# Kernel optimization log

Measured on AMD Instinct MI355X. Metric: run time of the kernel, lower is better.

Reference implementation:

```python
import jax, jax.numpy as jnp
import numpy as np

B, L, E, D, H, N_ENT = 64, 50, 50, 100, 100, 200000


def setup_inputs() -> dict:
    key = jax.random.key(0)
    ks = jax.random.split(key, 12)
    neighbor_ids = jax.random.randint(ks[0], (B, L, E), 0, N_ENT)
    # 0/1 adjacency; mimic GraphConstructer: symmetric with self-loops
    adj = jax.random.randint(ks[1], (B, L, E, E), 0, 2).astype(jnp.int32)
    adj = jnp.maximum(adj, adj.transpose(0, 1, 3, 2))
    adj = jnp.maximum(adj, jnp.eye(E, dtype=jnp.int32))
    s = 0.1  # ~ 1/sqrt(D) init scale
    emb = jax.random.normal(ks[2], (N_ENT, D), jnp.float32) * s
    Wq = jax.random.normal(ks[3], (D, H), jnp.float32) * s
    bq = jax.random.normal(ks[4], (H,), jnp.float32) * s
    Wk = jax.random.normal(ks[5], (D, H), jnp.float32) * s
    bk = jax.random.normal(ks[6], (H,), jnp.float32) * s
    Wv = jax.random.normal(ks[7], (D, H), jnp.float32) * s
    bv = jax.random.normal(ks[8], (H,), jnp.float32) * s
    Ws = jax.random.normal(ks[9], (D, H), jnp.float32) * s
    bs = jax.random.normal(ks[10], (H,), jnp.float32) * s
    return {"neighbor_ids": neighbor_ids, "adj": adj, "emb": emb,
            "Wq": Wq, "bq": bq, "Wk": Wk, "bk": bk,
            "Wv": Wv, "bv": bv, "Ws": Ws, "bs": bs}


def reference(neighbor_ids, adj, emb, Wq, bq, Wk, bk, Wv, bv, Ws, bs):
    b, l, e = neighbor_ids.shape
    d = emb.shape[1]
    h = Wq.shape[1]
    # embedding gather: [B,L,E,D] -> [G,E,D], G = B*L graphs
    x = emb[neighbor_ids].reshape(b * l, e, d)
    a = adj.reshape(b * l, e, e)
    # TransformerConv (heads=1): q,k,v linear with bias
    q = x @ Wq + bq
    k = x @ Wk + bk
    v = x @ Wv + bv
    scores = jnp.einsum('gid,gjd->gij', q, k) / jnp.sqrt(jnp.asarray(h, x.dtype))
    # edge (j -> i) exists when adj[j, i] != 0; target i attends over sources j
    mask = a.transpose(0, 2, 1) != 0  # mask[g, i, j]
    neg = jnp.finfo(scores.dtype).min
    attn = jax.nn.softmax(jnp.where(mask, scores, neg), axis=-1)
    # nodes with no incoming edge aggregate to zero (PyG softmax/scatter semantics)
    attn = jnp.where(mask.any(-1, keepdims=True), attn, jnp.zeros((), attn.dtype))
    agg = jnp.einsum('gij,gjd->gid', attn, v)
    out = agg + x @ Ws + bs  # root/skip connection with bias
    # take center node (index 0) of each ego-graph -> [B, L, H]
    return out.reshape(b, l, e, h)[:, :, 0, :]
```

## Files before the change

### kernel.cpp

```cpp
#include <hip/hip_runtime.h>
#include <math.h>

#define E_N 50
#define D_N 100
#define H_N 100
#define XSTR 51
#define NTHR 256
#define GATHER_IT ((E_N * (D_N / 4) + NTHR - 1) / NTHR)

__device__ __forceinline__ float bf2f(unsigned int s16) {
    return __uint_as_float(s16 << 16);
}

__device__ __forceinline__ unsigned short f2bf(float f) {
    unsigned int u = __float_as_uint(f);
    unsigned int r = (u + 0x7FFFu + ((u >> 16) & 1u)) >> 16;
    return (unsigned short)r;
}

template <bool F32>
__device__ __forceinline__ float ldx(const void* p, int i) {
    if (F32) return reinterpret_cast<const float*>(p)[i];
    return bf2f(reinterpret_cast<const unsigned short*>(p)[i]);
}

template <bool F32>
__device__ __forceinline__ float4 ld4(const void* p, long long i4) {
    if (F32) return reinterpret_cast<const float4*>(p)[i4];
    uint2 v = reinterpret_cast<const uint2*>(p)[i4];
    float4 f;
    f.x = bf2f(v.x & 0xFFFFu);
    f.y = bf2f(v.x >> 16);
    f.z = bf2f(v.y & 0xFFFFu);
    f.w = bf2f(v.y >> 16);
    return f;
}

template <bool F32>
__device__ __forceinline__ void graph_core(
    int g, int tid, int mk, const int* idr,
    const void* __restrict__ emb,
    const void* __restrict__ Wq, const void* __restrict__ bq,
    const void* __restrict__ Wk, const void* __restrict__ Wv,
    const void* __restrict__ bv, const void* __restrict__ Ws,
    const void* __restrict__ bs, void* __restrict__ out,
    float* xs, float* q0s, float* us, float* attns, float* ys, float* den_s)
{
    #pragma unroll
    for (int r = 0; r < GATHER_IT; ++r) {
        int i = tid + NTHR * r;
        if (i < E_N * (D_N / 4)) {
            int j  = i / 25;
            int d4 = i - j * 25;
            float4 v = ld4<F32>(emb, (long long)idr[r] * (D_N / 4) + d4);
            int d0 = d4 * 4;
            xs[(d0 + 0) * XSTR + j] = v.x;
            xs[(d0 + 1) * XSTR + j] = v.y;
            xs[(d0 + 2) * XSTR + j] = v.z;
            xs[(d0 + 3) * XSTR + j] = v.w;
        }
    }
    __syncthreads();

    if (tid < H_N) {
        float acc = ldx<F32>(bq, tid);
        #pragma unroll 10
        for (int d = 0; d < D_N; ++d)
            acc = fmaf(xs[d * XSTR], ldx<F32>(Wq, d * H_N + tid), acc);
        q0s[tid] = acc;
    }
    __syncthreads();

    if (tid < D_N) {
        float a0 = 0.f, a1 = 0.f, a2 = 0.f, a3 = 0.f;
        const float4* q4 = reinterpret_cast<const float4*>(q0s);
        #pragma unroll 5
        for (int h4 = 0; h4 < H_N / 4; ++h4) {
            float4 w = ld4<F32>(Wk, (long long)tid * (H_N / 4) + h4);
            float4 q = q4[h4];
            a0 = fmaf(w.x, q.x, a0);
            a1 = fmaf(w.y, q.y, a1);
            a2 = fmaf(w.z, q.z, a2);
            a3 = fmaf(w.w, q.w, a3);
        }
        us[tid] = (a0 + a1) + (a2 + a3);
    }
    __syncthreads();

    if (tid < 64) {
        float s = 0.f;
        if (tid < E_N) {
            #pragma unroll 10
            for (int d = 0; d < D_N; ++d)
                s = fmaf(us[d], xs[d * XSTR + tid], s);
            s *= 0.1f;
        }
        bool live = (tid < E_N) && (mk != 0);
        float m = live ? s : -3.0e38f;
        #pragma unroll
        for (int off = 32; off; off >>= 1)
            m = fmaxf(m, __shfl_xor(m, off));
        float e = live ? __expf(s - m) : 0.f;
        float den = e;
        #pragma unroll
        for (int off = 32; off; off >>= 1)
            den += __shfl_xor(den, off);
        float inv = den > 0.f ? 1.0f / den : 0.f;
        if (tid < E_N) attns[tid] = e * inv;
        if (tid == 0)  *den_s = den;
    }
    __syncthreads();

    if (tid < D_N) {
        float acc = 0.f;
        #pragma unroll 10
        for (int j = 0; j < E_N; ++j)
            acc = fmaf(attns[j], xs[tid * XSTR + j], acc);
        ys[tid] = acc;
    }
    __syncthreads();

    if (tid < H_N) {
        float sflag = *den_s > 0.f ? 1.f : 0.f;
        float acc = ldx<F32>(bs, tid) + ldx<F32>(bv, tid) * sflag;
        #pragma unroll 8
        for (int d = 0; d < D_N; ++d) {
            acc = fmaf(ys[d],        ldx<F32>(Wv, d * H_N + tid), acc);
            acc = fmaf(xs[d * XSTR], ldx<F32>(Ws, d * H_N + tid), acc);
        }
        size_t o = (size_t)g * H_N + tid;
        if (F32) reinterpret_cast<float*>(out)[o] = acc;
        else     reinterpret_cast<unsigned short*>(out)[o] = f2bf(acc);
    }
}

__global__ __launch_bounds__(NTHR, 7)
void graph_enc_kernel(const int* __restrict__ nbr,
                      const int* __restrict__ adj,
                      const void* __restrict__ emb,
                      const void* __restrict__ Wq, const void* __restrict__ bq,
                      const void* __restrict__ Wk, const void* __restrict__ Wv,
                      const void* __restrict__ bv, const void* __restrict__ Ws,
                      const void* __restrict__ bs, void* __restrict__ out)
{
    const int g = blockIdx.x;
    const int tid = threadIdx.x;

    __shared__ __align__(16) float xs[D_N * XSTR];
    __shared__ __align__(16) float q0s[H_N];
    __shared__ __align__(16) float us[D_N];
    __shared__ __align__(16) float attns[E_N];
    __shared__ __align__(16) float ys[D_N];
    __shared__ float den_s;
    __shared__ int   is_f32_s;

    int mk = 0;
    if (tid < E_N) mk = adj[(size_t)g * (E_N * E_N) + tid * E_N];

    int idr[GATHER_IT];
    #pragma unroll
    for (int r = 0; r < GATHER_IT; ++r) {
        int i = tid + NTHR * r;
        idr[r] = (i < E_N * (D_N / 4)) ? nbr[g * E_N + i / 25] : 0;
    }

    if (tid < 64) {
        unsigned short hw = reinterpret_cast<const unsigned short*>(emb)[tid * 2];
        float v = bf2f(hw);
        float a = fabsf(v);
        int sane = (v == 0.f) || (a >= 1e-4f && a <= 8.0f);
        unsigned long long ball = __ballot(sane);
        if (tid == 0) is_f32_s = (__popcll(ball) < 32) ? 1 : 0;
    }
    __syncthreads();

    if (is_f32_s)
        graph_core<true >(g, tid, mk, idr, emb, Wq, bq, Wk, Wv, bv, Ws, bs, out,
                          xs, q0s, us, attns, ys, &den_s);
    else
        graph_core<false>(g, tid, mk, idr, emb, Wq, bq, Wk, Wv, bv, Ws, bs, out,
                          xs, q0s, us, attns, ys, &den_s);
}

extern "C" void kernel_launch(void* const* d_in, const int* in_sizes, int n_in,
                              void* d_out, int out_size, void* d_ws, size_t ws_size,
                              hipStream_t stream) {
    const int* nbr = (const int*)d_in[0];
    const int* adj = (const int*)d_in[1];
    const void* emb = d_in[2];
    const void* Wq  = d_in[3];
    const void* bq  = d_in[4];
    const void* Wk  = d_in[5];
    const void* Wv  = d_in[7];
    const void* bv  = d_in[8];
    const void* Ws  = d_in[9];
    const void* bs  = d_in[10];

    const int G = in_sizes[0] / E_N;
    graph_enc_kernel<<<G, NTHR, 0, stream>>>(nbr, adj, emb, Wq, bq, Wk,
                                             Wv, bv, Ws, bs, d_out);
}
```

Before: 190.3 us.

## Split graph encoder into precompute and batched projection kernels

Precomputes Wk·Wq^T and Wk·bq once, so the per-graph query/key projection collapses to a single matrix-vector product on the center-node embedding. The center-node projections and the skip and value projections are batched over eight graphs per block, reusing each weight load across graphs. The work is spread over four kernel launches that pass intermediates through workspace memory. This cuts redundant weight traffic per graph but adds launch overhead and global round-trips for the intermediates.

```diff
diff --git a/kernel.cpp b/kernel.cpp
--- a/kernel.cpp
+++ b/kernel.cpp
@@ -5,8 +5,9 @@
 #define D_N 100
 #define H_N 100
 #define XSTR 51
+#define GT 8
 #define NTHR 256
-#define GATHER_IT ((E_N * (D_N / 4) + NTHR - 1) / NTHR)
+#define GATHER_IT 5
 
 __device__ __forceinline__ float bf2f(unsigned int s16) {
     return __uint_as_float(s16 << 16);
@@ -36,16 +37,153 @@
     return f;
 }
 
-template <bool F32>
-__device__ __forceinline__ void graph_core(
-    int g, int tid, int mk, const int* idr,
+__device__ __forceinline__ int sniff_f32(const void* emb, int tid, int* slot) {
+    if (tid < 64) {
+        unsigned short hw = reinterpret_cast<const unsigned short*>(emb)[tid * 2];
+        float v = bf2f(hw);
+        float a = fabsf(v);
+        int sane = (v == 0.f) || (a >= 1e-4f && a <= 8.0f);
+        unsigned long long ball = __ballot(sane);
+        if (tid == 0) *slot = (__popcll(ball) < 32) ? 1 : 0;
+    }
+    __syncthreads();
+    return *slot;
+}
+
+template <bool F32>
+__device__ __forceinline__ void precomp_core(
+    int dp, int tid, const void* __restrict__ Wq, const void* __restrict__ bq,
+    const void* __restrict__ Wk, float* __restrict__ At, float* __restrict__ c,
+    float* wq_s, float* bq_s)
+{
+    if (tid < H_N) wq_s[tid] = ldx<F32>(Wq, dp * H_N + tid);
+    if (dp == 0 && tid < H_N) bq_s[tid] = ldx<F32>(bq, tid);
+    __syncthreads();
+    if (tid < D_N) {
+        float a0 = 0.f, a1 = 0.f, a2 = 0.f, a3 = 0.f;
+        #pragma unroll
+        for (int h4 = 0; h4 < H_N / 4; ++h4) {
+            float4 w = ld4<F32>(Wk, (long long)tid * (H_N / 4) + h4);
+            a0 = fmaf(w.x, wq_s[h4 * 4 + 0], a0);
+            a1 = fmaf(w.y, wq_s[h4 * 4 + 1], a1);
+            a2 = fmaf(w.z, wq_s[h4 * 4 + 2], a2);
+            a3 = fmaf(w.w, wq_s[h4 * 4 + 3], a3);
+        }
+        At[dp * D_N + tid] = (a0 + a1) + (a2 + a3);
+        if (dp == 0) {
+            float c0 = 0.f, c1 = 0.f, c2 = 0.f, c3 = 0.f;
+            #pragma unroll
+            for (int h4 = 0; h4 < H_N / 4; ++h4) {
+                float4 w = ld4<F32>(Wk, (long long)tid * (H_N / 4) + h4);
+                c0 = fmaf(w.x, bq_s[h4 * 4 + 0], c0);
+                c1 = fmaf(w.y, bq_s[h4 * 4 + 1], c1);
+                c2 = fmaf(w.z, bq_s[h4 * 4 + 2], c2);
+                c3 = fmaf(w.w, bq_s[h4 * 4 + 3], c3);
+            }
+            c[tid] = (c0 + c1) + (c2 + c3);
+        }
+    }
+}
+
+__global__ __launch_bounds__(128)
+void precomp_kernel(const void* __restrict__ Wq, const void* __restrict__ bq,
+                    const void* __restrict__ Wk, const void* __restrict__ emb,
+                    float* __restrict__ At, float* __restrict__ c)
+{
+    __shared__ float wq_s[H_N];
+    __shared__ float bq_s[H_N];
+    __shared__ int is_f32_s;
+    int f32 = sniff_f32(emb, threadIdx.x, &is_f32_s);
+    if (f32) precomp_core<true >(blockIdx.x, threadIdx.x, Wq, bq, Wk, At, c, wq_s, bq_s);
+    else     precomp_core<false>(blockIdx.x, threadIdx.x, Wq, bq, Wk, At, c, wq_s, bq_s);
+}
+
+template <bool F32>
+__device__ __forceinline__ void ka_core(
+    int g0, int G, int tid,
+    const int* __restrict__ nbr, const void* __restrict__ emb,
+    const float* __restrict__ At, const float* __restrict__ c,
+    const void* __restrict__ Ws,
+    float* __restrict__ wl, float* __restrict__ skip, float* x0s)
+{
+    if (tid < GT * (D_N / 4)) {
+        int q = tid / (D_N / 4), d4 = tid - q * (D_N / 4);
+        int gq = g0 + q; if (gq >= G) gq = G - 1;
+        int id0 = nbr[gq * E_N];
+        float4 v = ld4<F32>(emb, (long long)id0 * (D_N / 4) + d4);
+        reinterpret_cast<float4*>(x0s + q * D_N)[d4] = v;
+    }
+    __syncthreads();
+
+    if (tid < D_N) {
+        int d = tid;
+        float cv = c[d];
+        float acc[GT];
+        #pragma unroll
+        for (int q = 0; q < GT; ++q) acc[q] = cv;
+        #pragma unroll 4
+        for (int dp = 0; dp < D_N; ++dp) {
+            float a = At[dp * D_N + d];
+            #pragma unroll
+            for (int q = 0; q < GT; ++q)
+                acc[q] = fmaf(a, x0s[q * D_N + dp], acc[q]);
+        }
+        #pragma unroll
+        for (int q = 0; q < GT; ++q) {
+            int gq = g0 + q;
+            if (gq < G) wl[(size_t)gq * D_N + d] = acc[q];
+        }
+    } else if (tid >= 128 && tid < 128 + H_N) {
+        int h = tid - 128;
+        float acc[GT];
+        #pragma unroll
+        for (int q = 0; q < GT; ++q) acc[q] = 0.f;
+        #pragma unroll 4
+        for (int d = 0; d < D_N; ++d) {
+            float w = ldx<F32>(Ws, d * H_N + h);
+            #pragma unroll
+            for (int q = 0; q < GT; ++q)
+                acc[q] = fmaf(w, x0s[q * D_N + d], acc[q]);
+        }
+        #pragma unroll
+        for (int q = 0; q < GT; ++q) {
+            int gq = g0 + q;
+            if (gq < G) skip[(size_t)gq * H_N + h] = acc[q];
+        }
+    }
+}
+
+__global__ __launch_bounds__(NTHR)
+void ka_kernel(const int* __restrict__ nbr, const void* __restrict__ emb,
+               const float* __restrict__ At, const float* __restrict__ c,
+               const void* __restrict__ Ws,
+               float* __restrict__ wl, float* __restrict__ skip, int G)
+{
+    __shared__ __align__(16) float x0s[GT * D_N];
+    __shared__ int is_f32_s;
+    int f32 = sniff_f32(emb, threadIdx.x, &is_f32_s);
+    if (f32) ka_core<true >(blockIdx.x * GT, G, threadIdx.x, nbr, emb, At, c, Ws, wl, skip, x0s);
+    else     ka_core<false>(blockIdx.x * GT, G, threadIdx.x, nbr, emb, At, c, Ws, wl, skip, x0s);
+}
+
+template <bool F32>
+__device__ __forceinline__ void kb_core(
+    int g, int tid,
+    const int* __restrict__ nbr, const int* __restrict__ adj,
     const void* __restrict__ emb,
-    const void* __restrict__ Wq, const void* __restrict__ bq,
-    const void* __restrict__ Wk, const void* __restrict__ Wv,
-    const void* __restrict__ bv, const void* __restrict__ Ws,
-    const void* __restrict__ bs, void* __restrict__ out,
-    float* xs, float* q0s, float* us, float* attns, float* ys, float* den_s)
-{
+    const float* __restrict__ wl, float* __restrict__ y, float* __restrict__ den,
+    float* xs, float* wls, float* ps)
+{
+    float wlv = (tid < D_N) ? wl[(size_t)g * D_N + tid] : 0.f;
+    int mk = (tid < E_N) ? adj[(size_t)g * (E_N * E_N) + tid * E_N] : 0;
+    int idr[GATHER_IT];
+    #pragma unroll
+    for (int r = 0; r < GATHER_IT; ++r) {
+        int i = tid + NTHR * r;
+        idr[r] = (i < E_N * (D_N / 4)) ? nbr[g * E_N + i / 25] : 0;
+    }
+    if (tid < D_N) wls[tid] = wlv;
+
     #pragma unroll
     for (int r = 0; r < GATHER_IT; ++r) {
         int i = tid + NTHR * r;
@@ -62,37 +200,12 @@
     }
     __syncthreads();
 
-    if (tid < H_N) {
-        float acc = ldx<F32>(bq, tid);
-        #pragma unroll 10
-        for (int d = 0; d < D_N; ++d)
-            acc = fmaf(xs[d * XSTR], ldx<F32>(Wq, d * H_N + tid), acc);
-        q0s[tid] = acc;
-    }
-    __syncthreads();
-
-    if (tid < D_N) {
-        float a0 = 0.f, a1 = 0.f, a2 = 0.f, a3 = 0.f;
-        const float4* q4 = reinterpret_cast<const float4*>(q0s);
-        #pragma unroll 5
-        for (int h4 = 0; h4 < H_N / 4; ++h4) {
-            float4 w = ld4<F32>(Wk, (long long)tid * (H_N / 4) + h4);
-            float4 q = q4[h4];
-            a0 = fmaf(w.x, q.x, a0);
-            a1 = fmaf(w.y, q.y, a1);
-            a2 = fmaf(w.z, q.z, a2);
-            a3 = fmaf(w.w, q.w, a3);
-        }
-        us[tid] = (a0 + a1) + (a2 + a3);
-    }
-    __syncthreads();
-
     if (tid < 64) {
         float s = 0.f;
         if (tid < E_N) {
             #pragma unroll 10
             for (int d = 0; d < D_N; ++d)
-                s = fmaf(us[d], xs[d * XSTR + tid], s);
+                s = fmaf(wls[d], xs[d * XSTR + tid], s);
             s *= 0.1f;
         }
         bool live = (tid < E_N) && (mk != 0);
@@ -101,13 +214,13 @@
         for (int off = 32; off; off >>= 1)
             m = fmaxf(m, __shfl_xor(m, off));
         float e = live ? __expf(s - m) : 0.f;
-        float den = e;
+        float dn = e;
         #pragma unroll
         for (int off = 32; off; off >>= 1)
-            den += __shfl_xor(den, off);
-        float inv = den > 0.f ? 1.0f / den : 0.f;
-        if (tid < E_N) attns[tid] = e * inv;
-        if (tid == 0)  *den_s = den;
+            dn += __shfl_xor(dn, off);
+        float inv = dn > 0.f ? 1.0f / dn : 0.f;
+        if (tid < E_N) ps[tid] = e * inv;
+        if (tid == 0)  den[g] = dn;
     }
     __syncthreads();
 
@@ -115,71 +228,90 @@
         float acc = 0.f;
         #pragma unroll 10
         for (int j = 0; j < E_N; ++j)
-            acc = fmaf(attns[j], xs[tid * XSTR + j], acc);
-        ys[tid] = acc;
-    }
-    __syncthreads();
-
-    if (tid < H_N) {
-        float sflag = *den_s > 0.f ? 1.f : 0.f;
-        float acc = ldx<F32>(bs, tid) + ldx<F32>(bv, tid) * sflag;
-        #pragma unroll 8
+            acc = fmaf(ps[j], xs[tid * XSTR + j], acc);
+        y[(size_t)g * D_N + tid] = acc;
+    }
+}
+
+__global__ __launch_bounds__(NTHR)
+void kb_kernel(const int* __restrict__ nbr, const int* __restrict__ adj,
+               const void* __restrict__ emb,
+               const float* __restrict__ wl, float* __restrict__ y,
+               float* __restrict__ den, int G)
+{
+    __shared__ __align__(16) float xs[D_N * XSTR];
+    __shared__ __align__(16) float wls[D_N];
+    __shared__ __align__(16) float ps[E_N];
+    __shared__ int is_f32_s;
+    int f32 = sniff_f32(emb, threadIdx.x, &is_f32_s);
+    if (f32) kb_core<true >(blockIdx.x, threadIdx.x, nbr, adj, emb, wl, y, den, xs, wls, ps);
+    else     kb_core<false>(blockIdx.x, threadIdx.x, nbr, adj, emb, wl, y, den, xs, wls, ps);
+}
+
+template <bool F32>
+__device__ __forceinline__ void kc_core(
+    int g0, int G, int tid,
+    const void* __restrict__ Wv, const void* __restrict__ bv,
+    const void* __restrict__ bs,
+    const float* __restrict__ skip, const float* __restrict__ y,
+    const float* __restrict__ den, void* __restrict__ out,
+    float* ys, float* denf)
+{
+    if (tid < GT * (D_N / 4)) {
+        int q = tid / (D_N / 4), d4 = tid - q * (D_N / 4);
+        int gq = g0 + q; if (gq >= G) gq = G - 1;
+        reinterpret_cast<float4*>(ys + q * D_N)[d4] =
+            reinterpret_cast<const float4*>(y + (size_t)gq * D_N)[d4];
+    }
+    if (tid < GT) {
+        int gq = g0 + tid; if (gq >= G) gq = G - 1;
+        denf[tid] = den[gq];
+    }
+    __syncthreads();
+
+    int half = tid >> 7;
+    int hh = tid & 127;
+    if (hh < H_N) {
+        int h = hh, qb = half * 4;
+        float b   = ldx<F32>(bs, h);
+        float bvv = ldx<F32>(bv, h);
+        float acc[4];
+        #pragma unroll
+        for (int q2 = 0; q2 < 4; ++q2) {
+            int gq = g0 + qb + q2; if (gq >= G) gq = G - 1;
+            acc[q2] = b + (denf[qb + q2] > 0.f ? bvv : 0.f) + skip[(size_t)gq * H_N + h];
+        }
+        #pragma unroll 4
         for (int d = 0; d < D_N; ++d) {
-            acc = fmaf(ys[d],        ldx<F32>(Wv, d * H_N + tid), acc);
-            acc = fmaf(xs[d * XSTR], ldx<F32>(Ws, d * H_N + tid), acc);
-        }
-        size_t o = (size_t)g * H_N + tid;
-        if (F32) reinterpret_cast<float*>(out)[o] = acc;
-        else     reinterpret_cast<unsigned short*>(out)[o] = f2bf(acc);
-    }
-}
-
-__global__ __launch_bounds__(NTHR, 7)
-void graph_enc_kernel(const int* __restrict__ nbr,
-                      const int* __restrict__ adj,
-                      const void* __restrict__ emb,
-                      const void* __restrict__ Wq, const void* __restrict__ bq,
-                      const void* __restrict__ Wk, const void* __restrict__ Wv,
-                      const void* __restrict__ bv, const void* __restrict__ Ws,
-                      const void* __restrict__ bs, void* __restrict__ out)
-{
-    const int g = blockIdx.x;
-    const int tid = threadIdx.x;
-
-    __shared__ __align__(16) float xs[D_N * XSTR];
-    __shared__ __align__(16) float q0s[H_N];
-    __shared__ __align__(16) float us[D_N];
-    __shared__ __align__(16) float attns[E_N];
-    __shared__ __align__(16) float ys[D_N];
-    __shared__ float den_s;
-    __shared__ int   is_f32_s;
-
-    int mk = 0;
-    if (tid < E_N) mk = adj[(size_t)g * (E_N * E_N) + tid * E_N];
-
-    int idr[GATHER_IT];
-    #pragma unroll
-    for (int r = 0; r < GATHER_IT; ++r) {
-        int i = tid + NTHR * r;
-        idr[r] = (i < E_N * (D_N / 4)) ? nbr[g * E_N + i / 25] : 0;
-    }
-
-    if (tid < 64) {
-        unsigned short hw = reinterpret_cast<const unsigned short*>(emb)[tid * 2];
-        float v = bf2f(hw);
-        float a = fabsf(v);
-        int sane = (v == 0.f) || (a >= 1e-4f && a <= 8.0f);
-        unsigned long long ball = __ballot(sane);
-        if (tid == 0) is_f32_s = (__popcll(ball) < 32) ? 1 : 0;
-    }
-    __syncthreads();
-
-    if (is_f32_s)
-        graph_core<true >(g, tid, mk, idr, emb, Wq, bq, Wk, Wv, bv, Ws, bs, out,
-                          xs, q0s, us, attns, ys, &den_s);
-    else
-        graph_core<false>(g, tid, mk, idr, emb, Wq, bq, Wk, Wv, bv, Ws, bs, out,
-                          xs, q0s, us, attns, ys, &den_s);
+            float w = ldx<F32>(Wv, d * H_N + h);
+            #pragma unroll
+            for (int q2 = 0; q2 < 4; ++q2)
+                acc[q2] = fmaf(w, ys[(qb + q2) * D_N + d], acc[q2]);
+        }
+        #pragma unroll
+        for (int q2 = 0; q2 < 4; ++q2) {
+            int gq = g0 + qb + q2;
+            if (gq < G) {
+                size_t o = (size_t)gq * H_N + h;
+                if (F32) reinterpret_cast<float*>(out)[o] = acc[q2];
+                else     reinterpret_cast<unsigned short*>(out)[o] = f2bf(acc[q2]);
+            }
+        }
+    }
+}
+
+__global__ __launch_bounds__(NTHR)
+void kc_kernel(const void* __restrict__ Wv, const void* __restrict__ bv,
+               const void* __restrict__ bs, const void* __restrict__ emb,
+               const float* __restrict__ skip, const float* __restrict__ y,
+               const float* __restrict__ den, void* __restrict__ out, int G)
+{
+    __shared__ __align__(16) float ys[GT * D_N];
+    __shared__ float denf[GT];
+    __shared__ int is_f32_s;
+    int f32 = sniff_f32(emb, threadIdx.x, &is_f32_s);
+    if (f32) kc_core<true >(blockIdx.x * GT, G, threadIdx.x, Wv, bv, bs, skip, y, den, out, ys, denf);
+    else     kc_core<false>(blockIdx.x * GT, G, threadIdx.x, Wv, bv, bs, skip, y, den, out, ys, denf);
 }
 
 extern "C" void kernel_launch(void* const* d_in, const int* in_sizes, int n_in,
@@ -197,6 +329,17 @@
     const void* bs  = d_in[10];
 
     const int G = in_sizes[0] / E_N;
-    graph_enc_kernel<<<G, NTHR, 0, stream>>>(nbr, adj, emb, Wq, bq, Wk,
-                                             Wv, bv, Ws, bs, d_out);
-}
+
+    float* At   = (float*)d_ws;
+    float* c    = At + D_N * D_N;
+    float* wl   = c + D_N;
+    float* skip = wl + (size_t)G * D_N;
+    float* y    = skip + (size_t)G * H_N;
+    float* den  = y + (size_t)G * D_N;
+
+    const int GB = (G + GT - 1) / GT;
+    precomp_kernel<<<D_N, 128, 0, stream>>>(Wq, bq, Wk, emb, At, c);
+    ka_kernel<<<GB, NTHR, 0, stream>>>(nbr, emb, At, c, Ws, wl, skip, G);
+    kb_kernel<<<G, NTHR, 0, stream>>>(nbr, adj, emb, wl, y, den, G);
+    kc_kernel<<<GB, NTHR, 0, stream>>>(Wv, bv, bs, emb, skip, y, den, d_out, G);
+}
```

After: 189.9 us. About the same (-0.2%).
